# Kernel tuning notes

Measured on AMD Instinct MI355X. Metric: run time of the kernel, lower is better.

Reference implementation:

```python
import jax, jax.numpy as jnp
import numpy as np

B, L, D = 2, 2048, 1024
H, DH = 16, 64
HIDDEN = 4096
DILATION, WINDOW, CAUSAL = 2, 512, True
EPS = 1e-5


def _ln(x, g, b):
    m = jnp.mean(x, axis=-1, keepdims=True)
    v = jnp.mean(jnp.square(x - m), axis=-1, keepdims=True)
    return (x - m) * jax.lax.rsqrt(v + EPS) * g + b


def setup_inputs() -> dict:
    key = jax.random.key(0)
    ks = jax.random.split(key, 8)
    s = 0.02
    return {
        "x": jax.random.normal(ks[0], (B, L, D), jnp.float32),
        "ln1_g": jnp.ones((D,), jnp.float32),
        "ln1_b": jnp.zeros((D,), jnp.float32),
        "w_qkv": jax.random.normal(ks[1], (3 * D, D), jnp.float32) * s,
        "b_qkv": jnp.zeros((3 * D,), jnp.float32),
        "w_o": jax.random.normal(ks[2], (D, D), jnp.float32) * s,
        "b_o": jnp.zeros((D,), jnp.float32),
        "ln2_g": jnp.ones((D,), jnp.float32),
        "ln2_b": jnp.zeros((D,), jnp.float32),
        "w_ff1": jax.random.normal(ks[3], (HIDDEN, D), jnp.float32) * s,
        "b_ff1": jnp.zeros((HIDDEN,), jnp.float32),
        "w_ff2": jax.random.normal(ks[4], (D, HIDDEN), jnp.float32) * s,
        "b_ff2": jnp.zeros((D,), jnp.float32),
    }


def reference(x, ln1_g, ln1_b, w_qkv, b_qkv, w_o, b_o, ln2_g, ln2_b, w_ff1, b_ff1, w_ff2, b_ff2):
    # pre-norm attention block with dilated/windowed/causal mask
    h = _ln(x, ln1_g, ln1_b)
    qkv = h @ w_qkv.T + b_qkv                      # [B, L, 3D]
    q, k, v = jnp.split(qkv, 3, axis=-1)
    q = q.reshape(B, L, H, DH)
    k = k.reshape(B, L, H, DH)
    v = v.reshape(B, L, H, DH)

    scale = 1.0 / jnp.sqrt(jnp.float32(DH))
    scores = jnp.einsum("bqhd,bkhd->bhqk", q, k) * scale  # [B, H, L, L]

    i = jnp.arange(L)[:, None]
    j = jnp.arange(L)[None, :]
    allowed = ((i - j) % DILATION == 0) & (jnp.abs(i - j) <= WINDOW)
    if CAUSAL:
        allowed = allowed & (j <= i)
    scores = jnp.where(allowed, scores, -jnp.inf)  # diagonal always allowed -> rows finite

    p = jax.nn.softmax(scores, axis=-1)
    attn = jnp.einsum("bhqk,bkhd->bqhd", p, v).reshape(B, L, D)

    out = x + attn @ w_o.T + b_o                   # residual 1 (dropout p=0)

    h2 = _ln(out, ln2_g, ln2_b)
    ff = jax.nn.gelu(h2 @ w_ff1.T + b_ff1, approximate=False) @ w_ff2.T + b_ff2
    return out + ff                                # residual 2
```

## Files before the change

### kernel.cpp

```cpp
#include <hip/hip_runtime.h>
#include <hip/hip_bf16.h>
#include <cmath>

#define Bsz 2
#define Lseq 2048
#define Dmod 1024
#define Hhead 16
#define DH 64
#define HID 4096
#define ROWS (Bsz * Lseq)
#define TD (3 * Dmod)

typedef __attribute__((ext_vector_type(8))) short bf16x8;
typedef __attribute__((ext_vector_type(4))) float f32x4;
typedef unsigned short ushort_t;

typedef const __attribute__((address_space(1))) void gv_t;
typedef __attribute__((address_space(3))) void lv_t;
#define GLDS16(GP, LP) __builtin_amdgcn_global_load_lds((gv_t*)(GP), (lv_t*)(LP), 16, 0, 0)

__device__ __forceinline__ float bf2f(short u)
{
    return __uint_as_float(((unsigned)(unsigned short)u) << 16);
}
__device__ __forceinline__ unsigned pack2(float a, float b)
{
    __hip_bfloat162 t;
    t.x = __float2bfloat16(a);
    t.y = __float2bfloat16(b);
    return *reinterpret_cast<unsigned*>(&t);
}
__device__ __forceinline__ float gelu_exact(float t)
{
    return 0.5f * t * (1.0f + erff(t * 0.70710678118654752f));
}

__device__ __forceinline__ void xcd_remap(int& mblk, int& nblk)
{
    int nx = gridDim.x;
    int nwg = nx * gridDim.y;
    int id = blockIdx.y * nx + blockIdx.x;
    int cpx = nwg >> 3;
    int swz = (id & 7) * cpx + (id >> 3);
    mblk = swz / nx;
    nblk = swz % nx;
}

__global__ __launch_bounds__(256) void f2b4_kernel(const float* __restrict__ s0, ushort_t* __restrict__ d0,
                                                   const float* __restrict__ s1, ushort_t* __restrict__ d1,
                                                   const float* __restrict__ s2, ushort_t* __restrict__ d2,
                                                   const float* __restrict__ s3, ushort_t* __restrict__ d3)
{
    int blk = blockIdx.x;
    const float* src;
    ushort_t* dst;
    int base;
    if (blk < 3072)      { src = s0; dst = d0; base = blk; }
    else if (blk < 4096) { src = s1; dst = d1; base = blk - 3072; }
    else if (blk < 8192) { src = s2; dst = d2; base = blk - 4096; }
    else                 { src = s3; dst = d3; base = blk - 8192; }
    int i = base * 256 + threadIdx.x;
    float4 v = reinterpret_cast<const float4*>(src)[i];
    uint2 o;
    o.x = pack2(v.x, v.y);
    o.y = pack2(v.z, v.w);
    reinterpret_cast<uint2*>(dst)[i] = o;
}

__global__ __launch_bounds__(256) void ln_kernel(const float* __restrict__ x,
                                                 const float* __restrict__ g,
                                                 const float* __restrict__ bta,
                                                 ushort_t* __restrict__ out)
{
    int row = blockIdx.x;
    int t = threadIdx.x;
    const float4* xr = reinterpret_cast<const float4*>(x) + (size_t)row * 256;
    float4 v = xr[t];
    float s  = v.x + v.y + v.z + v.w;
    float s2 = v.x * v.x + v.y * v.y + v.z * v.z + v.w * v.w;
#pragma unroll
    for (int o = 32; o > 0; o >>= 1) {
        s  += __shfl_down(s, o);
        s2 += __shfl_down(s2, o);
    }
    __shared__ float sa[4], sb[4];
    int wv = t >> 6, ln = t & 63;
    if (ln == 0) { sa[wv] = s; sb[wv] = s2; }
    __syncthreads();
    s  = sa[0] + sa[1] + sa[2] + sa[3];
    s2 = sb[0] + sb[1] + sb[2] + sb[3];
    float mean = s * (1.0f / 1024.0f);
    float var  = s2 * (1.0f / 1024.0f) - mean * mean;
    float inv  = rsqrtf(var + 1e-5f);
    float4 gv = reinterpret_cast<const float4*>(g)[t];
    float4 bv = reinterpret_cast<const float4*>(bta)[t];
    uint2 o;
    o.x = pack2((v.x - mean) * inv * gv.x + bv.x, (v.y - mean) * inv * gv.y + bv.y);
    o.y = pack2((v.z - mean) * inv * gv.z + bv.z, (v.w - mean) * inv * gv.w + bv.w);
    reinterpret_cast<uint2*>(out)[(size_t)row * 256 + t] = o;
}

__global__ __launch_bounds__(256) void gemm_bt(const ushort_t* __restrict__ A,
                                               const ushort_t* __restrict__ W,
                                               const float* __restrict__ bias,
                                               const float* __restrict__ res,
                                               void* __restrict__ C,
                                               int M, int N, int K, int ldw,
                                               int act, int obf)
{
    __shared__ ushort_t As0[128 * 64];
    __shared__ ushort_t Bs0[128 * 64];
    __shared__ ushort_t As1[128 * 64];
    __shared__ ushort_t Bs1[128 * 64];

    int tid = threadIdx.x;
    int w = tid >> 6, lane = tid & 63;
    int mblk, nblk;
    xcd_remap(mblk, nblk);
    int m0 = mblk * 128, n0 = nblk * 128;
    int wr = (w >> 1) * 64, wc = (w & 1) * 64;

    int srow = lane >> 3;
    int scol = (((lane & 7) ^ (lane >> 3)) & 7) * 8;
    const ushort_t* ga[4];
    const ushort_t* gb[4];
    int lofs[4];
#pragma unroll
    for (int q = 0; q < 4; ++q) {
        ga[q] = A + (size_t)(m0 + w * 32 + q * 8 + srow) * K + scol;
        gb[q] = W + (size_t)(n0 + w * 32 + q * 8 + srow) * ldw + scol;
        lofs[q] = (w * 32 + q * 8) * 64;
    }

    int fr = lane & 15;
    int fg = lane >> 4;
    int r0 = fg * 4;
    int cc = fr;

    f32x4 acc[4][4] = {};

    auto stage = [&](ushort_t* AS, ushort_t* BS, int k0) {
#pragma unroll
        for (int q = 0; q < 4; ++q) {
            GLDS16(ga[q] + k0, AS + lofs[q]);
            GLDS16(gb[q] + k0, BS + lofs[q]);
        }
    };
    auto compute = [&](const ushort_t* AS, const ushort_t* BS) {
#pragma unroll
        for (int kk = 0; kk < 2; ++kk) {
            bf16x8 af[4], bfr[4];
            int ca = ((kk * 4 + fg) ^ (fr & 7)) * 8;
#pragma unroll
            for (int i = 0; i < 4; ++i) {
                af[i]  = *reinterpret_cast<const bf16x8*>(&AS[(wr + i * 16 + fr) * 64 + ca]);
                bfr[i] = *reinterpret_cast<const bf16x8*>(&BS[(wc + i * 16 + fr) * 64 + ca]);
            }
#pragma unroll
            for (int mi = 0; mi < 4; ++mi)
#pragma unroll
                for (int ni = 0; ni < 4; ++ni)
                    acc[mi][ni] = __builtin_amdgcn_mfma_f32_16x16x32_bf16(
                        af[mi], bfr[ni], acc[mi][ni], 0, 0, 0);
        }
    };

    int nt = K >> 6;
    stage(As0, Bs0, 0);
    __syncthreads();
    for (int t = 0; t < nt; t += 2) {
        stage(As1, Bs1, (t + 1) * 64);
        compute(As0, Bs0);
        __syncthreads();
        if (t + 2 < nt) stage(As0, Bs0, (t + 2) * 64);
        compute(As1, Bs1);
        __syncthreads();
    }

    float bv[4];
#pragma unroll
    for (int ni = 0; ni < 4; ++ni)
        bv[ni] = bias ? bias[n0 + wc + ni * 16 + cc] : 0.0f;

#pragma unroll
    for (int mi = 0; mi < 4; ++mi) {
#pragma unroll
        for (int r = 0; r < 4; ++r) {
            int row = m0 + wr + mi * 16 + r0 + r;
            const float* resrow = res ? res + (size_t)row * N : nullptr;
#pragma unroll
            for (int ni = 0; ni < 4; ++ni) {
                int col = n0 + wc + ni * 16 + cc;
                float v = acc[mi][ni][r] + bv[ni];
                if (act == 1) v = gelu_exact(v);
                if (resrow) v += resrow[col];
                if (obf) {
                    reinterpret_cast<ushort_t*>(C)[(size_t)row * N + col] =
                        (ushort_t)__bfloat16_as_ushort(__float2bfloat16(v));
                } else {
                    reinterpret_cast<float*>(C)[(size_t)row * N + col] = v;
                }
            }
        }
    }
}

__global__ __launch_bounds__(256) void gemm_n64(const ushort_t* __restrict__ A,
                                                const ushort_t* __restrict__ W,
                                                const float* __restrict__ bias,
                                                const float* __restrict__ res,
                                                void* __restrict__ C,
                                                int M, int N, int K, int ldw,
                                                int act, int obf)
{
    __shared__ ushort_t As0[128 * 64];
    __shared__ ushort_t Bs0[64 * 64];
    __shared__ ushort_t As1[128 * 64];
    __shared__ ushort_t Bs1[64 * 64];

    int tid = threadIdx.x;
    int w = tid >> 6, lane = tid & 63;
    int mblk, nblk;
    xcd_remap(mblk, nblk);
    int m0 = mblk * 128, n0 = nblk * 64;
    int wr = (w >> 1) * 64, wc = (w & 1) * 32;

    int srow = lane >> 3;
    int scol = (((lane & 7) ^ (lane >> 3)) & 7) * 8;
    const ushort_t* ga[4];
    const ushort_t* gb[2];
    int laofs[4], lbofs[2];
#pragma unroll
    for (int q = 0; q < 4; ++q) {
        ga[q] = A + (size_t)(m0 + w * 32 + q * 8 + srow) * K + scol;
        laofs[q] = (w * 32 + q * 8) * 64;
    }
#pragma unroll
    for (int q = 0; q < 2; ++q) {
        gb[q] = W + (size_t)(n0 + w * 16 + q * 8 + srow) * ldw + scol;
        lbofs[q] = (w * 16 + q * 8) * 64;
    }

    int fr = lane & 15;
    int fg = lane >> 4;
    int r0 = fg * 4;
    int cc = fr;

    f32x4 acc[4][2] = {};

    auto stage = [&](ushort_t* AS, ushort_t* BS, int k0) {
#pragma unroll
        for (int q = 0; q < 4; ++q) GLDS16(ga[q] + k0, AS + laofs[q]);
#pragma unroll
        for (int q = 0; q < 2; ++q) GLDS16(gb[q] + k0, BS + lbofs[q]);
    };
    auto compute = [&](const ushort_t* AS, const ushort_t* BS) {
#pragma unroll
        for (int kk = 0; kk < 2; ++kk) {
            bf16x8 af[4], bfr[2];
            int ca = ((kk * 4 + fg) ^ (fr & 7)) * 8;
#pragma unroll
            for (int i = 0; i < 4; ++i)
                af[i] = *reinterpret_cast<const bf16x8*>(&AS[(wr + i * 16 + fr) * 64 + ca]);
#pragma unroll
            for (int i = 0; i < 2; ++i)
                bfr[i] = *reinterpret_cast<const bf16x8*>(&BS[(wc + i * 16 + fr) * 64 + ca]);
#pragma unroll
            for (int mi = 0; mi < 4; ++mi)
#pragma unroll
                for (int ni = 0; ni < 2; ++ni)
                    acc[mi][ni] = __builtin_amdgcn_mfma_f32_16x16x32_bf16(
                        af[mi], bfr[ni], acc[mi][ni], 0, 0, 0);
        }
    };

    int nt = K >> 6;
    stage(As0, Bs0, 0);
    __syncthreads();
    for (int t = 0; t < nt; t += 2) {
        stage(As1, Bs1, (t + 1) * 64);
        compute(As0, Bs0);
        __syncthreads();
        if (t + 2 < nt) stage(As0, Bs0, (t + 2) * 64);
        compute(As1, Bs1);
        __syncthreads();
    }

    float bv[2];
#pragma unroll
    for (int ni = 0; ni < 2; ++ni)
        bv[ni] = bias ? bias[n0 + wc + ni * 16 + cc] : 0.0f;

#pragma unroll
    for (int mi = 0; mi < 4; ++mi) {
#pragma unroll
        for (int r = 0; r < 4; ++r) {
            int row = m0 + wr + mi * 16 + r0 + r;
            const float* resrow = res ? res + (size_t)row * N : nullptr;
#pragma unroll
            for (int ni = 0; ni < 2; ++ni) {
                int col = n0 + wc + ni * 16 + cc;
                float v = acc[mi][ni][r] + bv[ni];
                if (act == 1) v = gelu_exact(v);
                if (resrow) v += resrow[col];
                if (obf) {
                    reinterpret_cast<ushort_t*>(C)[(size_t)row * N + col] =
                        (ushort_t)__bfloat16_as_ushort(__float2bfloat16(v));
                } else {
                    reinterpret_cast<float*>(C)[(size_t)row * N + col] = v;
                }
            }
        }
    }
}

__global__ __launch_bounds__(256) void attn_mfma(const ushort_t* __restrict__ qkv,
                                                 ushort_t* __restrict__ out)
{
    __shared__ ushort_t Vt[64][328];
    __shared__ ushort_t Pw[4][16][40];

    int bid = blockIdx.x;
    int qt = bid & 15, h = (bid >> 4) & 15, p = (bid >> 8) & 1, b = bid >> 9;
    int qt0 = qt * 64;
    int kstart = qt0 - 256;

    const ushort_t* base = qkv + (size_t)b * Lseq * TD;
    int tid = threadIdx.x;

#pragma unroll
    for (int it = 0; it < 10; ++it) {
        int idx = it * 256 + tid;
        int ko = idx >> 3;
        int dg = idx & 7;
        int kk = kstart + ko;
        bf16x8 v = {};
        if (kk >= 0)
            v = *reinterpret_cast<const bf16x8*>(base + (size_t)(2 * kk + p) * TD + 2048 + h * 64 + dg * 8);
#pragma unroll
        for (int j = 0; j < 8; ++j)
            Vt[dg * 8 + j][ko] = (ushort_t)v[j];
    }

    int w = tid >> 6, lane = tid & 63;
    int fr = lane & 15, fg = lane >> 4;
    int qw = qt0 + w * 16;
    const ushort_t* qrow = base + (size_t)(2 * (qw + fr) + p) * TD + h * 64;
    bf16x8 qf0 = *reinterpret_cast<const bf16x8*>(qrow + fg * 8);
    bf16x8 qf1 = *reinterpret_cast<const bf16x8*>(qrow + 32 + fg * 8);

    __syncthreads();

    float m[4]    = {-1e30f, -1e30f, -1e30f, -1e30f};
    float lsum[4] = {};
    f32x4 o[4]    = {};
    const float scale = 0.125f;
    int qbase = qw + fg * 4;

    for (int t = 0; t < 10; ++t) {
        int kt0 = kstart + t * 32;
        int kk0 = kt0 + fr, kk1 = kk0 + 16;
        int kk0c = kk0 < 0 ? 0 : kk0;
        int kk1c = kk1 < 0 ? 0 : kk1;
        const ushort_t* kr0 = base + (size_t)(2 * kk0c + p) * TD + 1024 + h * 64;
        const ushort_t* kr1 = base + (size_t)(2 * kk1c + p) * TD + 1024 + h * 64;
        bf16x8 k00 = *reinterpret_cast<const bf16x8*>(kr0 + fg * 8);
        bf16x8 k01 = *reinterpret_cast<const bf16x8*>(kr0 + 32 + fg * 8);
        bf16x8 k10 = *reinterpret_cast<const bf16x8*>(kr1 + fg * 8);
        bf16x8 k11 = *reinterpret_cast<const bf16x8*>(kr1 + 32 + fg * 8);

        f32x4 s0 = {}, s1 = {};
        s0 = __builtin_amdgcn_mfma_f32_16x16x32_bf16(qf0, k00, s0, 0, 0, 0);
        s0 = __builtin_amdgcn_mfma_f32_16x16x32_bf16(qf1, k01, s0, 0, 0, 0);
        s1 = __builtin_amdgcn_mfma_f32_16x16x32_bf16(qf0, k10, s1, 0, 0, 0);
        s1 = __builtin_amdgcn_mfma_f32_16x16x32_bf16(qf1, k11, s1, 0, 0, 0);

        int c0 = kt0 + fr, c1 = c0 + 16;
        float v0[4], v1[4], tmax[4];
#pragma unroll
        for (int r = 0; r < 4; ++r) {
            int qq = qbase + r;
            bool a0 = (c0 >= 0) && (c0 <= qq) && (c0 >= qq - 256);
            bool a1 = (c1 >= 0) && (c1 <= qq) && (c1 >= qq - 256);
            v0[r] = a0 ? s0[r] * scale : -1e30f;
            v1[r] = a1 ? s1[r] * scale : -1e30f;
            tmax[r] = fmaxf(v0[r], v1[r]);
        }
#pragma unroll
        for (int off = 1; off < 16; off <<= 1) {
#pragma unroll
            for (int r = 0; r < 4; ++r)
                tmax[r] = fmaxf(tmax[r], __shfl_xor(tmax[r], off));
        }
#pragma unroll
        for (int r = 0; r < 4; ++r) {
            float mn = fmaxf(m[r], tmax[r]);
            float corr = __expf(m[r] - mn);
            m[r] = mn;
            float p0 = __expf(v0[r] - mn);
            float p1 = __expf(v1[r] - mn);
            lsum[r] = lsum[r] * corr + p0 + p1;
#pragma unroll
            for (int db = 0; db < 4; ++db)
                o[db][r] *= corr;
            Pw[w][fg * 4 + r][fr]      = (ushort_t)__bfloat16_as_ushort(__float2bfloat16(p0));
            Pw[w][fg * 4 + r][fr + 16] = (ushort_t)__bfloat16_as_ushort(__float2bfloat16(p1));
        }

        bf16x8 pf = *reinterpret_cast<const bf16x8*>(&Pw[w][fr][fg * 8]);
#pragma unroll
        for (int db = 0; db < 4; ++db) {
            bf16x8 vf = *reinterpret_cast<const bf16x8*>(&Vt[db * 16 + fr][t * 32 + fg * 8]);
            o[db] = __builtin_amdgcn_mfma_f32_16x16x32_bf16(pf, vf, o[db], 0, 0, 0);
        }
    }

#pragma unroll
    for (int off = 1; off < 16; off <<= 1) {
#pragma unroll
        for (int r = 0; r < 4; ++r)
            lsum[r] += __shfl_xor(lsum[r], off);
    }
    float inv[4];
#pragma unroll
    for (int r = 0; r < 4; ++r) inv[r] = 1.0f / lsum[r];

#pragma unroll
    for (int r = 0; r < 4; ++r) {
        size_t orow = ((size_t)b * Lseq + 2 * (qbase + r) + p) * Dmod + h * 64;
#pragma unroll
        for (int db = 0; db < 4; ++db)
            out[orow + db * 16 + fr] =
                (ushort_t)__bfloat16_as_ushort(__float2bfloat16(o[db][r] * inv[r]));
    }
}

extern "C" void kernel_launch(void* const* d_in, const int* in_sizes, int n_in,
                              void* d_out, int out_size, void* d_ws, size_t ws_size,
                              hipStream_t stream)
{
    const float* x     = (const float*)d_in[0];
    const float* ln1_g = (const float*)d_in[1];
    const float* ln1_b = (const float*)d_in[2];
    const float* w_qkv = (const float*)d_in[3];
    const float* b_qkv = (const float*)d_in[4];
    const float* w_o   = (const float*)d_in[5];
    const float* b_o   = (const float*)d_in[6];
    const float* ln2_g = (const float*)d_in[7];
    const float* ln2_b = (const float*)d_in[8];
    const float* w_ff1 = (const float*)d_in[9];
    const float* b_ff1 = (const float*)d_in[10];
    const float* w_ff2 = (const float*)d_in[11];
    const float* b_ff2 = (const float*)d_in[12];
    float* out = (float*)d_out;

    ushort_t* wq     = (ushort_t*)d_ws;
    ushort_t* wo     = wq  + (size_t)TD * Dmod;
    ushort_t* wf1    = wo  + (size_t)Dmod * Dmod;
    ushort_t* wf2    = wf1 + (size_t)HID * Dmod;
    ushort_t* bufFF  = wf2 + (size_t)Dmod * HID;
    ushort_t* bufH   = bufFF + (size_t)ROWS * HID;
    ushort_t* bufAtt = bufH + (size_t)ROWS * Dmod;

    f2b4_kernel<<<12288, 256, 0, stream>>>(w_qkv, wq, w_o, wo, w_ff1, wf1, w_ff2, wf2);

    ln_kernel<<<ROWS, 256, 0, stream>>>(x, ln1_g, ln1_b, bufH);
    gemm_bt<<<dim3(TD / 128, ROWS / 128), 256, 0, stream>>>(bufH, wq, b_qkv, nullptr,
                                                            bufFF, ROWS, TD, Dmod, Dmod, 0, 1);
    attn_mfma<<<Bsz * 2 * Hhead * (1024 / 64), 256, 0, stream>>>(bufFF, bufAtt);
    gemm_n64<<<dim3(Dmod / 64, ROWS / 128), 256, 0, stream>>>(bufAtt, wo, b_o, x,
                                                              out, ROWS, Dmod, Dmod, Dmod, 0, 0);
    ln_kernel<<<ROWS, 256, 0, stream>>>(out, ln2_g, ln2_b, bufH);
    gemm_bt<<<dim3(HID / 128, ROWS / 128), 256, 0, stream>>>(bufH, wf1, b_ff1, nullptr,
                                                             bufFF, ROWS, HID, Dmod, Dmod, 1, 1);
    gemm_n64<<<dim3(Dmod / 64, ROWS / 128), 256, 0, stream>>>(bufFF, wf2, b_ff2, out,
                                                              out, ROWS, Dmod, HID, HID, 0, 0);
}
```

Before: 246.2 us.

## Keep two LDS stages in flight with partial vmcnt waits in GEMM loops

Restructures the double-buffered K loop of both GEMM kernels so that two tiles' global-to-LDS loads are outstanding at once. Each compute step waits only until the older stage's loads land (partial s_waitcnt vmcnt) rather than draining all memory ops with __syncthreads. It adds sched_barriers and a peeled epilogue. The vmcnt counts must exactly match the number of loads per stage, or the kernels will read LDS data that has not arrived yet.

```diff
diff --git a/kernel.cpp b/kernel.cpp
--- a/kernel.cpp
+++ b/kernel.cpp
@@ -167,15 +167,31 @@
 
     int nt = K >> 6;
     stage(As0, Bs0, 0);
-    __syncthreads();
-    for (int t = 0; t < nt; t += 2) {
-        stage(As1, Bs1, (t + 1) * 64);
+    stage(As1, Bs1, 64);
+    int t = 0;
+    for (; t + 3 < nt; t += 2) {
+        asm volatile("s_waitcnt vmcnt(8)" ::: "memory");
+        __builtin_amdgcn_s_barrier();
+        __builtin_amdgcn_sched_barrier(0);
         compute(As0, Bs0);
-        __syncthreads();
-        if (t + 2 < nt) stage(As0, Bs0, (t + 2) * 64);
+        __builtin_amdgcn_s_barrier();
+        stage(As0, Bs0, (t + 2) * 64);
+
+        asm volatile("s_waitcnt vmcnt(8)" ::: "memory");
+        __builtin_amdgcn_s_barrier();
+        __builtin_amdgcn_sched_barrier(0);
         compute(As1, Bs1);
-        __syncthreads();
-    }
+        __builtin_amdgcn_s_barrier();
+        stage(As1, Bs1, (t + 3) * 64);
+    }
+    asm volatile("s_waitcnt vmcnt(8)" ::: "memory");
+    __builtin_amdgcn_s_barrier();
+    __builtin_amdgcn_sched_barrier(0);
+    compute(As0, Bs0);
+    asm volatile("s_waitcnt vmcnt(0)" ::: "memory");
+    __builtin_amdgcn_s_barrier();
+    __builtin_amdgcn_sched_barrier(0);
+    compute(As1, Bs1);
 
     float bv[4];
 #pragma unroll
@@ -276,15 +292,31 @@
 
     int nt = K >> 6;
     stage(As0, Bs0, 0);
-    __syncthreads();
-    for (int t = 0; t < nt; t += 2) {
-        stage(As1, Bs1, (t + 1) * 64);
+    stage(As1, Bs1, 64);
+    int t = 0;
+    for (; t + 3 < nt; t += 2) {
+        asm volatile("s_waitcnt vmcnt(6)" ::: "memory");
+        __builtin_amdgcn_s_barrier();
+        __builtin_amdgcn_sched_barrier(0);
         compute(As0, Bs0);
-        __syncthreads();
-        if (t + 2 < nt) stage(As0, Bs0, (t + 2) * 64);
+        __builtin_amdgcn_s_barrier();
+        stage(As0, Bs0, (t + 2) * 64);
+
+        asm volatile("s_waitcnt vmcnt(6)" ::: "memory");
+        __builtin_amdgcn_s_barrier();
+        __builtin_amdgcn_sched_barrier(0);
         compute(As1, Bs1);
-        __syncthreads();
-    }
+        __builtin_amdgcn_s_barrier();
+        stage(As1, Bs1, (t + 3) * 64);
+    }
+    asm volatile("s_waitcnt vmcnt(6)" ::: "memory");
+    __builtin_amdgcn_s_barrier();
+    __builtin_amdgcn_sched_barrier(0);
+    compute(As0, Bs0);
+    asm volatile("s_waitcnt vmcnt(0)" ::: "memory");
+    __builtin_amdgcn_s_barrier();
+    __builtin_amdgcn_sched_barrier(0);
+    compute(As1, Bs1);
 
     float bv[2];
 #pragma unroll
```

Measured after the change: 236.0 us. -4.1%, faster.
